# Performance work log

Hardware: AMD Instinct MI355X
Metric: run time of the kernel (lower is better)

The kernel has to match this reference:

```python
import jax, jax.numpy as jnp
import numpy as np
import math

B, S, D = 2, 1024, 1024
H = 16
HD = D // H
E = 8
DFF = 4096
EPS = 1e-5


def _ln(x, g, b):
    m = jnp.mean(x, axis=-1, keepdims=True)
    v = jnp.mean((x - m) ** 2, axis=-1, keepdims=True)
    return (x - m) / jnp.sqrt(v + EPS) * g + b


def setup_inputs() -> dict:
    key = jax.random.key(0)
    ks = jax.random.split(key, 16)
    s = 0.02
    inp = {
        'src': jax.random.normal(ks[0], (B, S, D), jnp.float32),
        'qw': jax.random.normal(ks[1], (D, D), jnp.float32) * s,
        'kw': jax.random.normal(ks[2], (D, D), jnp.float32) * s,
        'vw': jax.random.normal(ks[3], (D, D), jnp.float32) * s,
        'ow': jax.random.normal(ks[4], (D, D), jnp.float32) * s,
        'gate_w': jax.random.normal(ks[5], (D, D), jnp.float32) * s,
        'gate_b': jax.random.normal(ks[6], (D,), jnp.float32) * s,
        'scale_w': jax.random.normal(ks[7], (H, HD), jnp.float32) * s,
        'n1_g': jnp.ones((D,), jnp.float32),
        'n1_b': jnp.zeros((D,), jnp.float32),
        'n2_g': jnp.ones((D,), jnp.float32),
        'n2_b': jnp.zeros((D,), jnp.float32),
        'moe_gate_w': jax.random.normal(ks[8], (D, E), jnp.float32) * s,
        'moe_gate_b': jnp.zeros((E,), jnp.float32),
        'w1': jax.random.normal(ks[9], (E, D, DFF), jnp.float32) * s,
        'b1': jnp.zeros((E, DFF), jnp.float32),
        'ln_g': jnp.ones((E, DFF), jnp.float32),
        'ln_b': jnp.zeros((E, DFF), jnp.float32),
        'w2': jax.random.normal(ks[10], (E, DFF, D), jnp.float32) * s,
        'b2': jnp.zeros((E, D), jnp.float32),
        'res_scale': jnp.ones((E,), jnp.float32),
    }
    return inp


def _forward(src, qw, kw, vw, ow, gate_w, gate_b, scale_w, n1_g, n1_b, n2_g, n2_b,
             moe_gate_w, moe_gate_b, w1, b1, ln_g, ln_b, w2, b2, res_scale):
    # ---- MemoAttention (non-flash path, eval: no dropout, no mask) ----
    q = (src @ qw).reshape(B, S, H, HD).transpose(0, 2, 1, 3)  # [B,H,S,HD]
    k = (src @ kw).reshape(B, S, H, HD).transpose(0, 2, 1, 3)
    v = (src @ vw).reshape(B, S, H, HD).transpose(0, 2, 1, 3)
    scores = jnp.einsum('bhqd,bhkd->bhqk', q, k) / math.sqrt(HD)
    # dynamic per-(head,query) scale gate
    scale = jax.nn.sigmoid(jnp.einsum('bhsd,hd->bhs', q, scale_w)) * 2.0
    scores = scores * scale[..., None]
    attn = jax.nn.softmax(scores, axis=-1)
    out = jnp.einsum('bhqk,bhkd->bhqd', attn, v)
    out = out.transpose(0, 2, 1, 3).reshape(B, S, D)
    gate = jax.nn.sigmoid(out @ gate_w + gate_b)
    attn_out = (out * gate) @ ow

    x = _ln(src + attn_out, n1_g, n1_b)

    # ---- MoE FFN (top-2 routing; eval: no gate noise; capacity never exceeded) ----
    xf = x.reshape(-1, D)                      # [T, D]
    T = xf.shape[0]
    logits = xf @ moe_gate_w + moe_gate_b      # [T, E]
    top_v, top_i = jax.lax.top_k(logits, 2)
    # NB: original sums BOTH top-k softmax weights per token (== 1.0), and the
    wsum = jnp.sum(jax.nn.softmax(top_v, axis=-1), axis=-1)   # [T] (== 1)
    e_sel = jnp.max(top_i, axis=-1)                           # [T]
    # dense per-expert FFN on all tokens, then per-token select (masked compute)
    h = jnp.einsum('td,edf->etf', xf, w1) + b1[:, None, :]    # [E,T,DFF]
    h = _ln(h, ln_g[:, None, :], ln_b[:, None, :])
    h = jax.nn.gelu(h, approximate=False)                     # torch nn.GELU (erf)
    y = jnp.einsum('etf,efd->etd', h, w2) + b2[:, None, :]    # [E,T,D]
    y = y * res_scale[:, None, None] + xf[None]
    sel = jnp.take_along_axis(y, e_sel[None, :, None], axis=0)[0]  # [T,D]
    moe_out = (sel * wsum[:, None]).reshape(B, S, D)

    return _ln(x + moe_out, n2_g, n2_b)


def reference(src, qw, kw, vw, ow, gate_w, gate_b, scale_w, n1_g, n1_b, n2_g, n2_b,
              moe_gate_w, moe_gate_b, w1, b1, ln_g, ln_b, w2, b2, res_scale):
    return _forward(src, qw, kw, vw, ow, gate_w, gate_b, scale_w, n1_g, n1_b,
                    n2_g, n2_b, moe_gate_w, moe_gate_b, w1, b1, ln_g, ln_b,
                    w2, b2, res_scale)
```

## Files before the change

### kernel.cpp

```cpp
#include <hip/hip_runtime.h>
#include <math.h>

#define TOK    2048
#define DMODEL 1024
#define NHEAD  16
#define HDIM   64
#define NEXP   8
#define DFFN   4096

typedef unsigned short u16;
typedef __attribute__((ext_vector_type(8))) short short8;
typedef __attribute__((ext_vector_type(4))) float floatx4;

__device__ __forceinline__ float sigmoidf_(float x) { return 1.f / (1.f + __expf(-x)); }

__device__ __forceinline__ u16 f2bf(float f) {
  union { float f; unsigned u; } v; v.f = f;
  unsigned r = v.u + 0x7FFFu + ((v.u >> 16) & 1u);
  return (u16)(r >> 16);
}
__device__ __forceinline__ float bf2f(u16 h) {
  union { unsigned u; float f; } v; v.u = ((unsigned)h) << 16; return v.f;
}

__device__ __forceinline__ void gload16(const void* g, void* l) {
  __builtin_amdgcn_global_load_lds((const __attribute__((address_space(1))) void*)g,
                                   (__attribute__((address_space(3))) void*)l, 16, 0, 0);
}

__device__ __forceinline__ float blockReduceSum256(float val) {
  __shared__ float ws_[4];
  #pragma unroll
  for (int off = 32; off; off >>= 1) val += __shfl_down(val, off);
  int lane = threadIdx.x & 63, w = threadIdx.x >> 6;
  if (lane == 0) ws_[w] = val;
  __syncthreads();
  float r = ws_[0] + ws_[1] + ws_[2] + ws_[3];
  __syncthreads();
  return r;
}

__global__ __launch_bounds__(256) void prep_kernel(
    const float* __restrict__ src, u16* __restrict__ Shi, u16* __restrict__ Slo,
    const float* __restrict__ Qw, const float* __restrict__ Kw, const float* __restrict__ Vw,
    u16* __restrict__ W3h, u16* __restrict__ W3l,
    const float* __restrict__ Gw, u16* __restrict__ Gh, u16* __restrict__ Gl,
    const float* __restrict__ Ow, u16* __restrict__ Oh, u16* __restrict__ Ol,
    const float* __restrict__ W1, u16* __restrict__ W1b) {
  const int bid = blockIdx.x, tid = threadIdx.x;
  __shared__ float tile[64][65];
  if (bid < 2048) {
    const int i = bid * 256 + tid;
    const float4 v = ((const float4*)src)[i];
    const float f[4] = {v.x, v.y, v.z, v.w};
    union { u16 s[4]; uint2 u; } h, l;
    #pragma unroll
    for (int j = 0; j < 4; ++j) {
      h.s[j] = f2bf(f[j]);
      l.s[j] = f2bf(f[j] - bf2f(h.s[j]));
    }
    ((uint2*)Shi)[i] = h.u;
    ((uint2*)Slo)[i] = l.u;
    return;
  }
  if (bid < 7168) {
    const float* W; u16 *Whp, *Wlp; int n0, k0;
    if (bid < 5120) {
      const int t = bid - 2048;
      const int z = t >> 5;
      const int zz = z >> 5;
      W = (zz == 0) ? Qw : (zz == 1) ? Kw : Vw;
      Whp = W3h + (size_t)zz * DMODEL * DMODEL;
      Wlp = W3l + (size_t)zz * DMODEL * DMODEL;
      n0 = (t & 31) * 32; k0 = (z & 31) * 32;
    } else {
      const int t = bid - 5120;
      const int t2 = t & 1023;
      if (t < 1024) { W = Gw; Whp = Gh; Wlp = Gl; }
      else          { W = Ow; Whp = Oh; Wlp = Ol; }
      n0 = (t2 & 31) * 32; k0 = (t2 >> 5) * 32;
    }
    const int r = tid >> 3, c4 = (tid & 7) * 4;
    const float4 v = *(const float4*)&W[(size_t)(k0 + r) * DMODEL + n0 + c4];
    tile[r][c4+0] = v.x; tile[r][c4+1] = v.y; tile[r][c4+2] = v.z; tile[r][c4+3] = v.w;
    __syncthreads();
    union { u16 s[4]; uint2 u; } h, l;
    #pragma unroll
    for (int j = 0; j < 4; ++j) {
      const float f = tile[c4 + j][r];
      h.s[j] = f2bf(f);
      l.s[j] = f2bf(f - bf2f(h.s[j]));
    }
    *(uint2*)&Whp[(size_t)(n0 + r) * DMODEL + k0 + c4] = h.u;
    *(uint2*)&Wlp[(size_t)(n0 + r) * DMODEL + k0 + c4] = l.u;
    return;
  }
  const int bid2 = bid - 7168;
  const int e = bid2 >> 10;
  const int rem = bid2 & 1023;
  const int n0 = (rem & 63) * 64;
  const int k0 = (rem >> 6) * 64;
  const float* W = W1 + (size_t)e * DMODEL * DFFN;
  u16* O = W1b + (size_t)e * DFFN * DMODEL;
  const int r = tid >> 2, c16 = (tid & 3) * 16;
  #pragma unroll
  for (int jj = 0; jj < 4; ++jj) {
    const float4 v = *(const float4*)&W[(size_t)(k0 + r) * DFFN + n0 + c16 + jj * 4];
    tile[r][c16 + jj*4 + 0] = v.x; tile[r][c16 + jj*4 + 1] = v.y;
    tile[r][c16 + jj*4 + 2] = v.z; tile[r][c16 + jj*4 + 3] = v.w;
  }
  __syncthreads();
  union { u16 s[8]; uint4 u; } o0, o1;
  #pragma unroll
  for (int j = 0; j < 8; ++j) o0.s[j] = f2bf(tile[c16 + j][r]);
  #pragma unroll
  for (int j = 0; j < 8; ++j) o1.s[j] = f2bf(tile[c16 + 8 + j][r]);
  *(uint4*)&O[(size_t)(n0 + r) * DMODEL + k0 + c16]     = o0.u;
  *(uint4*)&O[(size_t)(n0 + r) * DMODEL + k0 + c16 + 8] = o1.u;
}

template<int EPI, int TN>
__device__ __forceinline__ void gemm_split_body(
    u16* Ah, u16* Al, u16* Bh, u16* Bl, int bx, int by,
    const u16* __restrict__ Ahi, const u16* __restrict__ Alo,
    const u16* __restrict__ Whi, const u16* __restrict__ Wlo,
    const float* __restrict__ bias, const float* __restrict__ mul,
    float* __restrict__ Cf, u16* __restrict__ Chi, u16* __restrict__ Clo,
    u16* __restrict__ Vth, u16* __restrict__ Vtl,
    int M, int N, int K) {
  constexpr int NF = TN / 32;
  const int tid = threadIdx.x;
  const int lane = tid & 63, wave = tid >> 6;
  const int row0 = by * 128, col0 = bx * TN;
  const int wm = (wave & 1) * 64, wn = (wave >> 1) * (TN / 2);
  const int mr = tid >> 3;
  const int ksrc = (tid & 7) ^ ((tid >> 3) & 7);
  const floatx4 zero = {0.f, 0.f, 0.f, 0.f};
  floatx4 acc[4][NF];
  #pragma unroll
  for (int i = 0; i < 4; ++i)
    #pragma unroll
    for (int j = 0; j < NF; ++j) acc[i][j] = zero;

  for (int k0 = 0; k0 < K; k0 += 64) {
    __syncthreads();
    #pragma unroll
    for (int p = 0; p < 4; ++p) {
      const size_t ga = (size_t)(row0 + p * 32 + mr) * K + (k0 + ksrc * 8);
      const size_t off = (size_t)(p * 256 + wave * 64) * 16;
      gload16(Ahi + ga, (char*)Ah + off);
      gload16(Alo + ga, (char*)Al + off);
    }
    #pragma unroll
    for (int p = 0; p < NF; ++p) {
      const size_t gb = (size_t)(col0 + p * 32 + mr) * K + (k0 + ksrc * 8);
      const size_t off = (size_t)(p * 256 + wave * 64) * 16;
      gload16(Whi + gb, (char*)Bh + off);
      gload16(Wlo + gb, (char*)Bl + off);
    }
    __syncthreads();
    #pragma unroll
    for (int kk = 0; kk < 2; ++kk) {
      short8 ah[4], al[4], bh[NF], bl[NF];
      #pragma unroll
      for (int i = 0; i < 4; ++i) {
        const int ml = wm + i * 16 + (lane & 15);
        const int cm = (kk * 4 + (lane >> 4)) ^ (ml & 7);
        ah[i] = *(const short8*)&Ah[ml * 64 + cm * 8];
        al[i] = *(const short8*)&Al[ml * 64 + cm * 8];
      }
      #pragma unroll
      for (int j = 0; j < NF; ++j) {
        const int nl = wn + j * 16 + (lane & 15);
        const int cn = (kk * 4 + (lane >> 4)) ^ (nl & 7);
        bh[j] = *(const short8*)&Bh[nl * 64 + cn * 8];
        bl[j] = *(const short8*)&Bl[nl * 64 + cn * 8];
      }
      #pragma unroll
      for (int i = 0; i < 4; ++i)
        #pragma unroll
        for (int j = 0; j < NF; ++j) {
          acc[i][j] = __builtin_amdgcn_mfma_f32_16x16x32_bf16(ah[i], bh[j], acc[i][j], 0, 0, 0);
          acc[i][j] = __builtin_amdgcn_mfma_f32_16x16x32_bf16(al[i], bh[j], acc[i][j], 0, 0, 0);
          acc[i][j] = __builtin_amdgcn_mfma_f32_16x16x32_bf16(ah[i], bl[j], acc[i][j], 0, 0, 0);
        }
    }
  }
  const int cl = lane & 15, quad = lane >> 4;
  if (EPI == 2 && col0 >= 2048) {
    #pragma unroll
    for (int i = 0; i < 4; ++i)
      #pragma unroll
      for (int j = 0; j < NF; ++j) {
        const int dg = col0 + wn + j * 16 + cl - 2048;
        const int bh_ = dg >> 6, d = dg & 63;
        const int row = row0 + wm + i * 16 + quad * 4;
        const int b = row >> 10, t0 = row & 1023;
        union { u16 s[4]; uint2 u; } hh, ll;
        #pragma unroll
        for (int r = 0; r < 4; ++r) {
          const float v = acc[i][j][r];
          hh.s[r] = f2bf(v);
          ll.s[r] = f2bf(v - bf2f(hh.s[r]));
        }
        const size_t base = ((size_t)(b * 16 + bh_) * 64 + d) * 1024 + t0;
        *(uint2*)&Vth[base] = hh.u;
        *(uint2*)&Vtl[base] = ll.u;
      }
    return;
  }
  #pragma unroll
  for (int i = 0; i < 4; ++i)
    #pragma unroll
    for (int j = 0; j < NF; ++j) {
      const int col = col0 + wn + j * 16 + cl;
      #pragma unroll
      for (int r = 0; r < 4; ++r) {
        const int row = row0 + wm + i * 16 + quad * 4 + r;
        const float v = acc[i][j][r];
        if (EPI == 0) {
          Cf[(size_t)row * N + col] = v;
        } else if (EPI == 1) {
          const float s = sigmoidf_(v + bias[col]);
          const float g = s * mul[(size_t)row * N + col];
          const u16 hh = f2bf(g);
          Chi[(size_t)row * N + col] = hh;
          Clo[(size_t)row * N + col] = f2bf(g - bf2f(hh));
        } else {
          const u16 hh = f2bf(v);
          Chi[(size_t)row * N + col] = hh;
          Clo[(size_t)row * N + col] = f2bf(v - bf2f(hh));
        }
      }
    }
}

template<int EPI, int TN>
__global__ __launch_bounds__(256, TN == 64 ? 3 : 2) void gemm_split_kernel(
    const u16* __restrict__ Ahi, const u16* __restrict__ Alo,
    const u16* __restrict__ Whi, const u16* __restrict__ Wlo,
    const float* __restrict__ bias, const float* __restrict__ mul,
    float* __restrict__ Cf, u16* __restrict__ Chi, u16* __restrict__ Clo,
    u16* __restrict__ Vth, u16* __restrict__ Vtl,
    int M, int N, int K) {
  __shared__ u16 Ah[128*64], Al[128*64], Bh[TN*64], Bl[TN*64];
  gemm_split_body<EPI, TN>(Ah, Al, Bh, Bl, blockIdx.x, blockIdx.y,
      Ahi, Alo, Whi, Wlo, bias, mul, Cf, Chi, Clo, Vth, Vtl, M, N, K);
}

struct GemmShared { u16 Ah[128*64]; u16 Al[128*64]; u16 Bh[64*64]; u16 Bl[64*64]; };
template<int EPI>
__global__ __launch_bounds__(256, 3) void gemm_split_w2_kernel(
    const u16* __restrict__ Ahi, const u16* __restrict__ Alo,
    const u16* __restrict__ Whi, const u16* __restrict__ Wlo,
    const float* __restrict__ bias, const float* __restrict__ mul,
    float* __restrict__ Cf, u16* __restrict__ Chi, u16* __restrict__ Clo,
    const float* __restrict__ W2, u16* __restrict__ W2b, int khalf) {
  __shared__ union { GemmShared g; float tile[32][33]; } sm;
  const int bid = blockIdx.x;
  if (bid < 256) {
    gemm_split_body<EPI, 64>(sm.g.Ah, sm.g.Al, sm.g.Bh, sm.g.Bl, bid & 15, bid >> 4,
        Ahi, Alo, Whi, Wlo, bias, mul, Cf, Chi, Clo, nullptr, nullptr,
        TOK, DMODEL, DMODEL);
    return;
  }
  const int t = bid - 256;
  const int e = t >> 5, n0 = (t & 31) * 32;
  const float* W = W2 + (size_t)e * DFFN * DMODEL;
  u16* O = W2b + (size_t)e * DMODEL * DFFN;
  const int r = threadIdx.x >> 3, c4 = (threadIdx.x & 7) * 4;
  for (int kt = 0; kt < 64; ++kt) {
    const int k0 = khalf * 2048 + kt * 32;
    __syncthreads();
    const float4 v = *(const float4*)&W[(size_t)(k0 + r) * DMODEL + n0 + c4];
    sm.tile[r][c4+0] = v.x; sm.tile[r][c4+1] = v.y;
    sm.tile[r][c4+2] = v.z; sm.tile[r][c4+3] = v.w;
    __syncthreads();
    union { u16 s[4]; uint2 u; } h4;
    #pragma unroll
    for (int j = 0; j < 4; ++j) h4.s[j] = f2bf(sm.tile[c4 + j][r]);
    *(uint2*)&O[(size_t)(n0 + r) * DFFN + k0 + c4] = h4.u;
  }
}

template<int EPI, int TN>
__global__ __launch_bounds__(256, TN == 64 ? 4 : 3) void gemm_moe_kernel(
    const u16* __restrict__ A, const u16* __restrict__ Wt,
    const float* __restrict__ bias,
    const int* __restrict__ perm, const int* __restrict__ offs,
    const int* __restrict__ counts,
    u16* __restrict__ Hout, float* __restrict__ P0, float* __restrict__ P1,
    int N, int K) {
  constexpr int NF = TN / 32;
  const int z = blockIdx.z;
  const int e = (EPI == 0) ? z : (z & 7);
  const int ks = (EPI == 0) ? 0 : (z >> 3);
  const int ne = counts[e];
  const int tm = blockIdx.y;
  if (tm * 128 >= ne) return;
  const int kbeg = (EPI == 0) ? 0 : ks * (K >> 1);
  const int kend = (EPI == 0) ? K : kbeg + (K >> 1);
  __shared__ u16 As_[128*64], Bs_[TN*64];
  __shared__ int toks[128];
  const int tid = threadIdx.x;
  if (tid < 128) {
    const int idx = tm * 128 + tid;
    toks[tid] = perm[offs[e] + (idx < ne ? idx : 0)];
  }
  __syncthreads();
  const int lane = tid & 63, wave = tid >> 6;
  const int wm = (wave & 1) * 64, wn = (wave >> 1) * (TN / 2);
  const int mr = tid >> 3;
  const int ksrc = (tid & 7) ^ ((tid >> 3) & 7);
  size_t abase[4];
  #pragma unroll
  for (int p = 0; p < 4; ++p) abase[p] = (size_t)toks[p * 32 + mr] * K;
  const u16* We = Wt + (size_t)e * N * K;
  const int col0 = blockIdx.x * TN;
  const floatx4 zero = {0.f, 0.f, 0.f, 0.f};
  floatx4 acc[4][NF];
  #pragma unroll
  for (int i = 0; i < 4; ++i)
    #pragma unroll
    for (int j = 0; j < NF; ++j) acc[i][j] = zero;

  for (int k0 = kbeg; k0 < kend; k0 += 64) {
    __syncthreads();
    #pragma unroll
    for (int p = 0; p < 4; ++p) {
      const size_t off = (size_t)(p * 256 + wave * 64) * 16;
      gload16(A + abase[p] + (k0 + ksrc * 8), (char*)As_ + off);
    }
    #pragma unroll
    for (int p = 0; p < NF; ++p) {
      const size_t off = (size_t)(p * 256 + wave * 64) * 16;
      gload16(We + (size_t)(col0 + p * 32 + mr) * K + (k0 + ksrc * 8), (char*)Bs_ + off);
    }
    __syncthreads();
    #pragma unroll
    for (int kk = 0; kk < 2; ++kk) {
      short8 a[4], b[NF];
      #pragma unroll
      for (int i = 0; i < 4; ++i) {
        const int ml = wm + i * 16 + (lane & 15);
        const int cm = (kk * 4 + (lane >> 4)) ^ (ml & 7);
        a[i] = *(const short8*)&As_[ml * 64 + cm * 8];
      }
      #pragma unroll
      for (int j = 0; j < NF; ++j) {
        const int nl = wn + j * 16 + (lane & 15);
        const int cn = (kk * 4 + (lane >> 4)) ^ (nl & 7);
        b[j] = *(const short8*)&Bs_[nl * 64 + cn * 8];
      }
      #pragma unroll
      for (int i = 0; i < 4; ++i)
        #pragma unroll
        for (int j = 0; j < NF; ++j)
          acc[i][j] = __builtin_amdgcn_mfma_f32_16x16x32_bf16(a[i], b[j], acc[i][j], 0, 0, 0);
    }
  }
  const int cl = lane & 15, quad = lane >> 4;
  float* Pp = (EPI == 1) ? (ks ? P1 : P0) : nullptr;
  #pragma unroll
  for (int i = 0; i < 4; ++i)
    #pragma unroll
    for (int j = 0; j < NF; ++j) {
      const int col = col0 + wn + j * 16 + cl;
      #pragma unroll
      for (int r = 0; r < 4; ++r) {
        const int rl = wm + i * 16 + quad * 4 + r;
        if (tm * 128 + rl < ne) {
          const int tok = toks[rl];
          if (EPI == 0)
            Hout[(size_t)tok * N + col] = f2bf(acc[i][j][r] + bias[(size_t)e * N + col]);
          else
            Pp[(size_t)tok * N + col] = acc[i][j][r];
        }
      }
    }
}

__global__ __launch_bounds__(512, 2) void attn_mfma_kernel(
    const u16* __restrict__ QKh, const u16* __restrict__ QKl,
    const u16* __restrict__ Vth, const u16* __restrict__ Vtl,
    const float* __restrict__ scale_w,
    float* __restrict__ AOf, u16* __restrict__ AOh, u16* __restrict__ AOl) {
  const int qt = blockIdx.x, h = blockIdx.y, b = blockIdx.z;
  __shared__ u16 Kh[64*64], Kl[64*64], Vh[64*64], Vl[64*64];
  __shared__ u16 Ph[8][16*40], Pl[8][16*40];
  const int tid = threadIdx.x, lane = tid & 63, wave = tid >> 6;
  const int i15 = lane & 15, quad = lane >> 4;
  const floatx4 zero = {0.f, 0.f, 0.f, 0.f};

  short8 qh[2], ql[2];
  const size_t qrow = ((size_t)b * 1024 + qt * 128 + wave * 16 + i15) * 3072 + h * 64;
  #pragma unroll
  for (int kk = 0; kk < 2; ++kk) {
    qh[kk] = *(const short8*)&QKh[qrow + kk * 32 + quad * 8];
    ql[kk] = *(const short8*)&QKl[qrow + kk * 32 + quad * 8];
  }
  float dot = 0.f;
  #pragma unroll
  for (int kk = 0; kk < 2; ++kk)
    #pragma unroll
    for (int j = 0; j < 8; ++j) {
      const float sw = scale_w[h * 64 + kk * 32 + quad * 8 + j];
      dot += (bf2f((u16)qh[kk][j]) + bf2f((u16)ql[kk][j])) * sw;
    }
  dot += __shfl_xor(dot, 16);
  dot += __shfl_xor(dot, 32);
  const float g = 2.f * sigmoidf_(dot) * 0.125f;
  float stot[4];
  #pragma unroll
  for (int r = 0; r < 4; ++r) stot[r] = __shfl(g, (lane >> 4) * 4 + r);

  float m_r[4], l_r[4];
  floatx4 Of[4];
  #pragma unroll
  for (int r = 0; r < 4; ++r) { m_r[r] = -1e30f; l_r[r] = 0.f; }
  #pragma unroll
  for (int f = 0; f < 4; ++f) Of[f] = zero;
  u16* PhW = Ph[wave];
  u16* PlW = Pl[wave];

  const int sr = tid >> 3;
  const int sc = ((tid & 7) ^ (sr & 7)) * 8;
  for (int kt = 0; kt < 16; ++kt) {
    __syncthreads();
    {
      const size_t off = (size_t)wave * 1024;
      const size_t kg = ((size_t)b * 1024 + kt * 64 + sr) * 3072 + 1024 + h * 64 + sc;
      gload16(QKh + kg, (char*)Kh + off);
      gload16(QKl + kg, (char*)Kl + off);
      const size_t vg = ((size_t)(b * 16 + h) * 64 + sr) * 1024 + kt * 64 + sc;
      gload16(Vth + vg, (char*)Vh + off);
      gload16(Vtl + vg, (char*)Vl + off);
    }
    __syncthreads();
    float pm[4][4];
    #pragma unroll
    for (int jn = 0; jn < 4; ++jn) {
      floatx4 a = zero;
      #pragma unroll
      for (int kk = 0; kk < 2; ++kk) {
        const int n = jn * 16 + i15;
        const int ch = ((kk * 4 + quad) ^ (n & 7)) * 8;
        const short8 bh = *(const short8*)&Kh[n * 64 + ch];
        const short8 bl = *(const short8*)&Kl[n * 64 + ch];
        a = __builtin_amdgcn_mfma_f32_16x16x32_bf16(qh[kk], bh, a, 0, 0, 0);
        a = __builtin_amdgcn_mfma_f32_16x16x32_bf16(ql[kk], bh, a, 0, 0, 0);
        a = __builtin_amdgcn_mfma_f32_16x16x32_bf16(qh[kk], bl, a, 0, 0, 0);
      }
      #pragma unroll
      for (int r = 0; r < 4; ++r) pm[jn][r] = a[r] * stot[r];
    }
    float alpha[4];
    #pragma unroll
    for (int r = 0; r < 4; ++r) {
      float mx = fmaxf(fmaxf(pm[0][r], pm[1][r]), fmaxf(pm[2][r], pm[3][r]));
      mx = fmaxf(mx, __shfl_xor(mx, 1));
      mx = fmaxf(mx, __shfl_xor(mx, 2));
      mx = fmaxf(mx, __shfl_xor(mx, 4));
      mx = fmaxf(mx, __shfl_xor(mx, 8));
      const float mn = fmaxf(m_r[r], mx);
      alpha[r] = __expf(m_r[r] - mn);
      m_r[r] = mn;
      float rs = 0.f;
      #pragma unroll
      for (int jn = 0; jn < 4; ++jn) { pm[jn][r] = __expf(pm[jn][r] - mn); rs += pm[jn][r]; }
      rs += __shfl_xor(rs, 1);
      rs += __shfl_xor(rs, 2);
      rs += __shfl_xor(rs, 4);
      rs += __shfl_xor(rs, 8);
      l_r[r] = l_r[r] * alpha[r] + rs;
    }
    #pragma unroll
    for (int f = 0; f < 4; ++f)
      #pragma unroll
      for (int r = 0; r < 4; ++r) Of[f][r] *= alpha[r];
    #pragma unroll
    for (int kk = 0; kk < 2; ++kk) {
      #pragma unroll
      for (int jj = 0; jj < 2; ++jj) {
        const int jn = kk * 2 + jj;
        #pragma unroll
        for (int r = 0; r < 4; ++r) {
          const int a = (quad * 4 + r) * 40 + jj * 16 + i15;
          const u16 hh = f2bf(pm[jn][r]);
          PhW[a] = hh;
          PlW[a] = f2bf(pm[jn][r] - bf2f(hh));
        }
      }
      const short8 pah = *(const short8*)&PhW[i15 * 40 + quad * 8];
      const short8 pal = *(const short8*)&PlW[i15 * 40 + quad * 8];
      #pragma unroll
      for (int f = 0; f < 4; ++f) {
        const int d = f * 16 + i15;
        const int ch = ((kk * 4 + quad) ^ (d & 7)) * 8;
        const short8 vbh = *(const short8*)&Vh[d * 64 + ch];
        const short8 vbl = *(const short8*)&Vl[d * 64 + ch];
        Of[f] = __builtin_amdgcn_mfma_f32_16x16x32_bf16(pah, vbh, Of[f], 0, 0, 0);
        Of[f] = __builtin_amdgcn_mfma_f32_16x16x32_bf16(pal, vbh, Of[f], 0, 0, 0);
        Of[f] = __builtin_amdgcn_mfma_f32_16x16x32_bf16(pah, vbl, Of[f], 0, 0, 0);
      }
    }
  }
  float inv[4];
  #pragma unroll
  for (int r = 0; r < 4; ++r) inv[r] = 1.f / l_r[r];
  #pragma unroll
  for (int f = 0; f < 4; ++f)
    #pragma unroll
    for (int r = 0; r < 4; ++r) {
      const size_t row = (size_t)b * 1024 + qt * 128 + wave * 16 + quad * 4 + r;
      const int col = h * 64 + f * 16 + i15;
      const float val = Of[f][r] * inv[r];
      AOf[row * 1024 + col] = val;
      const u16 hh = f2bf(val);
      AOh[row * 1024 + col] = hh;
      AOl[row * 1024 + col] = f2bf(val - bf2f(hh));
    }
}

__global__ __launch_bounds__(256) void ln_add_router_kernel(
    const float* __restrict__ A, const float* __restrict__ Bp,
    const float* __restrict__ g, const float* __restrict__ beta,
    float* __restrict__ outf, u16* __restrict__ outh,
    const float* __restrict__ gw, const float* __restrict__ gb,
    int* __restrict__ e_sel) {
  __shared__ float xrow[DMODEL];
  int t = blockIdx.x, tid = threadIdx.x;
  const float* a = A + (size_t)t * DMODEL;
  const float* b = Bp + (size_t)t * DMODEL;
  float v[4]; float s = 0.f;
  #pragma unroll
  for (int i = 0; i < 4; ++i) { int d = tid + i*256; v[i] = a[d] + b[d]; s += v[i]; }
  s = blockReduceSum256(s);
  float mean = s * (1.f/1024.f);
  float q = 0.f;
  #pragma unroll
  for (int i = 0; i < 4; ++i) { float df = v[i]-mean; q += df*df; }
  q = blockReduceSum256(q);
  float rstd = rsqrtf(q*(1.f/1024.f) + 1e-5f);
  #pragma unroll
  for (int i = 0; i < 4; ++i) {
    int d = tid + i*256;
    float val = (v[i]-mean)*rstd*g[d] + beta[d];
    outf[(size_t)t*DMODEL + d] = val;
    outh[(size_t)t*DMODEL + d] = f2bf(val);
    xrow[d] = val;
  }
  __syncthreads();
  if (tid < 64) {
    float acc[NEXP] = {};
    for (int d = tid; d < DMODEL; d += 64) {
      float xv = xrow[d];
      const float* gr = gw + (size_t)d * NEXP;
      #pragma unroll
      for (int e = 0; e < NEXP; ++e) acc[e] += xv * gr[e];
    }
    #pragma unroll
    for (int e = 0; e < NEXP; ++e) {
      #pragma unroll
      for (int off = 32; off; off >>= 1) acc[e] += __shfl_down(acc[e], off);
    }
    if (tid == 0) {
      float lg[NEXP];
      #pragma unroll
      for (int e = 0; e < NEXP; ++e) lg[e] = acc[e] + gb[e];
      int i1 = 0;
      for (int e = 1; e < NEXP; ++e) if (lg[e] > lg[i1]) i1 = e;
      int i2 = -1;
      for (int e = 0; e < NEXP; ++e) {
        if (e == i1) continue;
        if (i2 < 0 || lg[e] > lg[i2]) i2 = e;
      }
      e_sel[t] = (i1 > i2) ? i1 : i2;
    }
  }
}

__global__ __launch_bounds__(256) void ln_final_kernel(
    const float* __restrict__ X, const float* __restrict__ P0,
    const float* __restrict__ P1, const float* __restrict__ B2,
    const float* __restrict__ rsv, const int* __restrict__ e_sel,
    const float* __restrict__ g, const float* __restrict__ beta,
    float* __restrict__ out) {
  int t = blockIdx.x, tid = threadIdx.x;
  const int e = e_sel[t];
  const float rse = rsv[e];
  const float* b2e = B2 + (size_t)e * DMODEL;
  const int d0 = tid * 4;
  const size_t base = (size_t)t * DMODEL + d0;
  const float4 xv = *(const float4*)&X[base];
  const float4 p0v = *(const float4*)&P0[base];
  const float4 p1v = *(const float4*)&P1[base];
  const float4 bv = *(const float4*)&b2e[d0];
  float v[4]; float s = 0.f;
  v[0] = 2.f*xv.x + (p0v.x + p1v.x + bv.x) * rse;
  v[1] = 2.f*xv.y + (p0v.y + p1v.y + bv.y) * rse;
  v[2] = 2.f*xv.z + (p0v.z + p1v.z + bv.z) * rse;
  v[3] = 2.f*xv.w + (p0v.w + p1v.w + bv.w) * rse;
  s = v[0] + v[1] + v[2] + v[3];
  s = blockReduceSum256(s);
  float mean = s * (1.f/1024.f);
  float q = 0.f;
  #pragma unroll
  for (int i = 0; i < 4; ++i) { float df = v[i]-mean; q += df*df; }
  q = blockReduceSum256(q);
  float rstd = rsqrtf(q*(1.f/1024.f) + 1e-5f);
  const float4 g4 = *(const float4*)&g[d0];
  const float4 be4 = *(const float4*)&beta[d0];
  float4 o;
  o.x = (v[0]-mean)*rstd*g4.x + be4.x;
  o.y = (v[1]-mean)*rstd*g4.y + be4.y;
  o.z = (v[2]-mean)*rstd*g4.z + be4.z;
  o.w = (v[3]-mean)*rstd*g4.w + be4.w;
  *(float4*)&out[base] = o;
}

__global__ __launch_bounds__(256) void moe_group_kernel(
    const int* __restrict__ e_sel, int* __restrict__ perm,
    int* __restrict__ g_offs, int* __restrict__ g_counts) {
  __shared__ int cnt[NEXP], offs[NEXP], cur[NEXP];
  int tid = threadIdx.x;
  if (tid < NEXP) cnt[tid] = 0;
  __syncthreads();
  for (int t = tid; t < TOK; t += 256) atomicAdd(&cnt[e_sel[t]], 1);
  __syncthreads();
  if (tid == 0) {
    int run = 0;
    for (int e = 0; e < NEXP; ++e) { offs[e] = run; cur[e] = run; run += cnt[e]; }
  }
  __syncthreads();
  if (tid < NEXP) { g_offs[tid] = offs[tid]; g_counts[tid] = cnt[tid]; }
  for (int t = tid; t < TOK; t += 256) {
    int pos = atomicAdd(&cur[e_sel[t]], 1);
    perm[pos] = t;
  }
}

__global__ __launch_bounds__(256) void moe_ln_gelu_kernel(
    u16* __restrict__ H, const float* __restrict__ ln_g,
    const float* __restrict__ ln_b, const int* __restrict__ e_sel) {
  int t = blockIdx.x, tid = threadIdx.x;
  int e = e_sel[t];
  u16* hp = H + (size_t)t * DFFN;
  float v[16]; float s = 0.f;
  #pragma unroll
  for (int i = 0; i < 4; ++i) {
    const int d = i * 1024 + tid * 4;
    union { uint2 u; u16 q[4]; } hv;
    hv.u = *(const uint2*)&hp[d];
    #pragma unroll
    for (int j = 0; j < 4; ++j) { v[i*4+j] = bf2f(hv.q[j]); s += v[i*4+j]; }
  }
  s = blockReduceSum256(s);
  float mean = s * (1.f/4096.f);
  float q = 0.f;
  #pragma unroll
  for (int i = 0; i < 16; ++i) { float df = v[i]-mean; q += df*df; }
  q = blockReduceSum256(q);
  float rstd = rsqrtf(q*(1.f/4096.f) + 1e-5f);
  const float* gg = ln_g + (size_t)e * DFFN;
  const float* bb = ln_b + (size_t)e * DFFN;
  #pragma unroll
  for (int i = 0; i < 4; ++i) {
    const int d = i * 1024 + tid * 4;
    const float4 g4 = *(const float4*)&gg[d];
    const float4 b4 = *(const float4*)&bb[d];
    const float gf[4] = {g4.x, g4.y, g4.z, g4.w};
    const float bf[4] = {b4.x, b4.y, b4.z, b4.w};
    union { uint2 u; u16 q[4]; } ov;
    #pragma unroll
    for (int j = 0; j < 4; ++j) {
      float xx = (v[i*4+j]-mean)*rstd*gf[j] + bf[j];
      ov.q[j] = f2bf(0.5f * xx * (1.f + erff(xx * 0.7071067811865475f)));
    }
    *(uint2*)&hp[d] = ov.u;
  }
}

extern "C" void kernel_launch(void* const* d_in, const int* in_sizes, int n_in,
                              void* d_out, int out_size, void* d_ws, size_t ws_size,
                              hipStream_t stream) {
  (void)in_sizes; (void)n_in; (void)out_size; (void)ws_size;
  const float* src    = (const float*)d_in[0];
  const float* qw     = (const float*)d_in[1];
  const float* kw     = (const float*)d_in[2];
  const float* vw     = (const float*)d_in[3];
  const float* ow     = (const float*)d_in[4];
  const float* gate_w = (const float*)d_in[5];
  const float* gate_b = (const float*)d_in[6];
  const float* scale_w= (const float*)d_in[7];
  const float* n1_g   = (const float*)d_in[8];
  const float* n1_b   = (const float*)d_in[9];
  const float* n2_g   = (const float*)d_in[10];
  const float* n2_b   = (const float*)d_in[11];
  const float* mgw    = (const float*)d_in[12];
  const float* mgb    = (const float*)d_in[13];
  const float* w1     = (const float*)d_in[14];
  const float* b1     = (const float*)d_in[15];
  const float* ln_g   = (const float*)d_in[16];
  const float* ln_b   = (const float*)d_in[17];
  const float* w2     = (const float*)d_in[18];
  const float* b2     = (const float*)d_in[19];
  const float* rs     = (const float*)d_in[20];

  char* ws = (char*)d_ws;
  const size_t MB = 1024 * 1024;
  u16*   src_hi = (u16*)(ws + 0*MB);
  u16*   src_lo = (u16*)(ws + 4*MB);
  u16*   Wt3_hi = (u16*)(ws + 8*MB);
  u16*   Wt3_lo = (u16*)(ws + 14*MB);
  u16*   gw_hi  = (u16*)(ws + 20*MB);
  u16*   gw_lo  = (u16*)(ws + 22*MB);
  u16*   ow_hi  = (u16*)(ws + 24*MB);
  u16*   ow_lo  = (u16*)(ws + 26*MB);
  u16*   W1A    = (u16*)(ws + 28*MB);
  u16*   W2A    = (u16*)(ws + 92*MB);
  u16*   qkv_hi = (u16*)(ws + 156*MB);
  u16*   qkv_lo = (u16*)(ws + 168*MB);
  u16*   Vt_hi  = (u16*)(ws + 180*MB);
  u16*   Vt_lo  = (u16*)(ws + 184*MB);
  float* ao     = (float*)(ws + 188*MB);
  u16*   ao_hi  = (u16*)(ws + 196*MB);
  u16*   ao_lo  = (u16*)(ws + 200*MB);
  u16*   gb_hi  = (u16*)(ws + 204*MB);
  u16*   gb_lo  = (u16*)(ws + 208*MB);
  float* proj   = (float*)(ws + 212*MB);
  float* x      = (float*)(ws + 220*MB);
  u16*   x_hi   = (u16*)(ws + 228*MB);
  u16*   h      = (u16*)(ws + 232*MB);
  float* p0     = (float*)(ws + 248*MB);
  float* p1     = (float*)(ws + 256*MB);
  int*   e_sel  = (int*)(ws + 264*MB);
  int*   perm   = e_sel + TOK;
  int*   offs   = perm + TOK;
  int*   cnts   = offs + NEXP;

  dim3 blk(256);

  prep_kernel<<<15360, blk, 0, stream>>>(src, src_hi, src_lo,
      qw, kw, vw, Wt3_hi, Wt3_lo, gate_w, gw_hi, gw_lo, ow, ow_hi, ow_lo,
      w1, W1A);

  gemm_split_kernel<2,64><<<dim3(48,16), blk, 0, stream>>>(src_hi, src_lo,
      Wt3_hi, Wt3_lo, nullptr, nullptr, nullptr, qkv_hi, qkv_lo, Vt_hi, Vt_lo,
      TOK, 3072, DMODEL);

  attn_mfma_kernel<<<dim3(8, NHEAD, 2), dim3(512), 0, stream>>>(
      qkv_hi, qkv_lo, Vt_hi, Vt_lo, scale_w, ao, ao_hi, ao_lo);

  gemm_split_w2_kernel<1><<<512, blk, 0, stream>>>(ao_hi, ao_lo, gw_hi, gw_lo,
      gate_b, ao, nullptr, gb_hi, gb_lo, w2, W2A, 0);

  gemm_split_w2_kernel<0><<<512, blk, 0, stream>>>(gb_hi, gb_lo, ow_hi, ow_lo,
      nullptr, nullptr, proj, nullptr, nullptr, w2, W2A, 1);

  ln_add_router_kernel<<<TOK, blk, 0, stream>>>(src, proj, n1_g, n1_b, x, x_hi,
      mgw, mgb, e_sel);

  moe_group_kernel<<<1, blk, 0, stream>>>(e_sel, perm, offs, cnts);

  gemm_moe_kernel<0,128><<<dim3(DFFN/128, 16, 8), blk, 0, stream>>>(
      x_hi, W1A, b1, perm, offs, cnts, h, nullptr, nullptr, DFFN, DMODEL);

  moe_ln_gelu_kernel<<<TOK, blk, 0, stream>>>(h, ln_g, ln_b, e_sel);

  gemm_moe_kernel<1,64><<<dim3(DMODEL/64, 16, 16), blk, 0, stream>>>(
      h, W2A, nullptr, perm, offs, cnts, nullptr, p0, p1, DMODEL, DFFN);

  ln_final_kernel<<<TOK, blk, 0, stream>>>(x, p0, p1, b2, rs, e_sel, n2_g, n2_b,
      (float*)d_out);
}
```

Baseline: 713.3 us.

## Shrink gate/out-proj GEMM tiles to 64x64 and retile W1 transpose

Templates the split-bf16 GEMM body on the M tile and uses 64x64 tiles for the gate and output projection GEMMs. This doubles their block count to 512 (768 including the fused W2 conversion blocks), which improves CU fill on a 2048x1024 output. It also raises the launch bound to 4 blocks per CU and sets the QKV GEMM bound to 3. Separately, it reorganises the W1 transpose/convert blocks so global reads are row-coalesced and writes are 16-byte stores per thread. Smaller tiles reduce data reuse per block, and the tighter launch bounds may force register spilling.

```diff
diff --git a/kernel.cpp b/kernel.cpp
--- a/kernel.cpp
+++ b/kernel.cpp
@@ -102,24 +102,32 @@
   const int k0 = (rem >> 6) * 64;
   const float* W = W1 + (size_t)e * DMODEL * DFFN;
   u16* O = W1b + (size_t)e * DFFN * DMODEL;
-  const int r = tid >> 2, c16 = (tid & 3) * 16;
-  #pragma unroll
-  for (int jj = 0; jj < 4; ++jj) {
-    const float4 v = *(const float4*)&W[(size_t)(k0 + r) * DFFN + n0 + c16 + jj * 4];
-    tile[r][c16 + jj*4 + 0] = v.x; tile[r][c16 + jj*4 + 1] = v.y;
-    tile[r][c16 + jj*4 + 2] = v.z; tile[r][c16 + jj*4 + 3] = v.w;
+  {
+    const int lr = tid >> 4;
+    const int lc = (tid & 15) * 4;
+    #pragma unroll
+    for (int p = 0; p < 4; ++p) {
+      const float4 v = *(const float4*)&W[(size_t)(k0 + p * 16 + lr) * DFFN + n0 + lc];
+      tile[p*16 + lr][lc+0] = v.x; tile[p*16 + lr][lc+1] = v.y;
+      tile[p*16 + lr][lc+2] = v.z; tile[p*16 + lr][lc+3] = v.w;
+    }
   }
   __syncthreads();
-  union { u16 s[8]; uint4 u; } o0, o1;
-  #pragma unroll
-  for (int j = 0; j < 8; ++j) o0.s[j] = f2bf(tile[c16 + j][r]);
-  #pragma unroll
-  for (int j = 0; j < 8; ++j) o1.s[j] = f2bf(tile[c16 + 8 + j][r]);
-  *(uint4*)&O[(size_t)(n0 + r) * DMODEL + k0 + c16]     = o0.u;
-  *(uint4*)&O[(size_t)(n0 + r) * DMODEL + k0 + c16 + 8] = o1.u;
-}
-
-template<int EPI, int TN>
+  {
+    const int kl = (tid & 7) * 8;
+    const int nl = tid >> 3;
+    #pragma unroll
+    for (int q = 0; q < 2; ++q) {
+      const int n = q * 32 + nl;
+      union { u16 s[8]; uint4 u; } o;
+      #pragma unroll
+      for (int j = 0; j < 8; ++j) o.s[j] = f2bf(tile[kl + j][n]);
+      *(uint4*)&O[(size_t)(n0 + n) * DMODEL + k0 + kl] = o.u;
+    }
+  }
+}
+
+template<int EPI, int TM, int TN>
 __device__ __forceinline__ void gemm_split_body(
     u16* Ah, u16* Al, u16* Bh, u16* Bl, int bx, int by,
     const u16* __restrict__ Ahi, const u16* __restrict__ Alo,
@@ -128,24 +136,25 @@
     float* __restrict__ Cf, u16* __restrict__ Chi, u16* __restrict__ Clo,
     u16* __restrict__ Vth, u16* __restrict__ Vtl,
     int M, int N, int K) {
+  constexpr int MI = TM / 32;
   constexpr int NF = TN / 32;
   const int tid = threadIdx.x;
   const int lane = tid & 63, wave = tid >> 6;
-  const int row0 = by * 128, col0 = bx * TN;
-  const int wm = (wave & 1) * 64, wn = (wave >> 1) * (TN / 2);
+  const int row0 = by * TM, col0 = bx * TN;
+  const int wm = (wave & 1) * (TM / 2), wn = (wave >> 1) * (TN / 2);
   const int mr = tid >> 3;
   const int ksrc = (tid & 7) ^ ((tid >> 3) & 7);
   const floatx4 zero = {0.f, 0.f, 0.f, 0.f};
-  floatx4 acc[4][NF];
-  #pragma unroll
-  for (int i = 0; i < 4; ++i)
+  floatx4 acc[MI][NF];
+  #pragma unroll
+  for (int i = 0; i < MI; ++i)
     #pragma unroll
     for (int j = 0; j < NF; ++j) acc[i][j] = zero;
 
   for (int k0 = 0; k0 < K; k0 += 64) {
     __syncthreads();
     #pragma unroll
-    for (int p = 0; p < 4; ++p) {
+    for (int p = 0; p < MI; ++p) {
       const size_t ga = (size_t)(row0 + p * 32 + mr) * K + (k0 + ksrc * 8);
       const size_t off = (size_t)(p * 256 + wave * 64) * 16;
       gload16(Ahi + ga, (char*)Ah + off);
@@ -161,9 +170,9 @@
     __syncthreads();
     #pragma unroll
     for (int kk = 0; kk < 2; ++kk) {
-      short8 ah[4], al[4], bh[NF], bl[NF];
-      #pragma unroll
-      for (int i = 0; i < 4; ++i) {
+      short8 ah[MI], al[MI], bh[NF], bl[NF];
+      #pragma unroll
+      for (int i = 0; i < MI; ++i) {
         const int ml = wm + i * 16 + (lane & 15);
         const int cm = (kk * 4 + (lane >> 4)) ^ (ml & 7);
         ah[i] = *(const short8*)&Ah[ml * 64 + cm * 8];
@@ -177,7 +186,7 @@
         bl[j] = *(const short8*)&Bl[nl * 64 + cn * 8];
       }
       #pragma unroll
-      for (int i = 0; i < 4; ++i)
+      for (int i = 0; i < MI; ++i)
         #pragma unroll
         for (int j = 0; j < NF; ++j) {
           acc[i][j] = __builtin_amdgcn_mfma_f32_16x16x32_bf16(ah[i], bh[j], acc[i][j], 0, 0, 0);
@@ -189,7 +198,7 @@
   const int cl = lane & 15, quad = lane >> 4;
   if (EPI == 2 && col0 >= 2048) {
     #pragma unroll
-    for (int i = 0; i < 4; ++i)
+    for (int i = 0; i < MI; ++i)
       #pragma unroll
       for (int j = 0; j < NF; ++j) {
         const int dg = col0 + wn + j * 16 + cl - 2048;
@@ -210,7 +219,7 @@
     return;
   }
   #pragma unroll
-  for (int i = 0; i < 4; ++i)
+  for (int i = 0; i < MI; ++i)
     #pragma unroll
     for (int j = 0; j < NF; ++j) {
       const int col = col0 + wn + j * 16 + cl;
@@ -236,7 +245,7 @@
 }
 
 template<int EPI, int TN>
-__global__ __launch_bounds__(256, TN == 64 ? 3 : 2) void gemm_split_kernel(
+__global__ __launch_bounds__(256, 3) void gemm_split_kernel(
     const u16* __restrict__ Ahi, const u16* __restrict__ Alo,
     const u16* __restrict__ Whi, const u16* __restrict__ Wlo,
     const float* __restrict__ bias, const float* __restrict__ mul,
@@ -244,27 +253,28 @@
     u16* __restrict__ Vth, u16* __restrict__ Vtl,
     int M, int N, int K) {
   __shared__ u16 Ah[128*64], Al[128*64], Bh[TN*64], Bl[TN*64];
-  gemm_split_body<EPI, TN>(Ah, Al, Bh, Bl, blockIdx.x, blockIdx.y,
+  gemm_split_body<EPI, 128, TN>(Ah, Al, Bh, Bl, blockIdx.x, blockIdx.y,
       Ahi, Alo, Whi, Wlo, bias, mul, Cf, Chi, Clo, Vth, Vtl, M, N, K);
 }
 
-struct GemmShared { u16 Ah[128*64]; u16 Al[128*64]; u16 Bh[64*64]; u16 Bl[64*64]; };
+struct GemmShared64 { u16 Ah[64*64]; u16 Al[64*64]; u16 Bh[64*64]; u16 Bl[64*64]; };
 template<int EPI>
-__global__ __launch_bounds__(256, 3) void gemm_split_w2_kernel(
+__global__ __launch_bounds__(256, 4) void gemm_split_w2_kernel(
     const u16* __restrict__ Ahi, const u16* __restrict__ Alo,
     const u16* __restrict__ Whi, const u16* __restrict__ Wlo,
     const float* __restrict__ bias, const float* __restrict__ mul,
     float* __restrict__ Cf, u16* __restrict__ Chi, u16* __restrict__ Clo,
     const float* __restrict__ W2, u16* __restrict__ W2b, int khalf) {
-  __shared__ union { GemmShared g; float tile[32][33]; } sm;
+  __shared__ union { GemmShared64 g; float tile[32][33]; } sm;
   const int bid = blockIdx.x;
-  if (bid < 256) {
-    gemm_split_body<EPI, 64>(sm.g.Ah, sm.g.Al, sm.g.Bh, sm.g.Bl, bid & 15, bid >> 4,
+  if (bid < 512) {
+    gemm_split_body<EPI, 64, 64>(sm.g.Ah, sm.g.Al, sm.g.Bh, sm.g.Bl,
+        bid & 15, bid >> 4,
         Ahi, Alo, Whi, Wlo, bias, mul, Cf, Chi, Clo, nullptr, nullptr,
         TOK, DMODEL, DMODEL);
     return;
   }
-  const int t = bid - 256;
+  const int t = bid - 512;
   const int e = t >> 5, n0 = (t & 31) * 32;
   const float* W = W2 + (size_t)e * DFFN * DMODEL;
   u16* O = W2b + (size_t)e * DMODEL * DFFN;
@@ -752,10 +762,10 @@
   attn_mfma_kernel<<<dim3(8, NHEAD, 2), dim3(512), 0, stream>>>(
       qkv_hi, qkv_lo, Vt_hi, Vt_lo, scale_w, ao, ao_hi, ao_lo);
 
-  gemm_split_w2_kernel<1><<<512, blk, 0, stream>>>(ao_hi, ao_lo, gw_hi, gw_lo,
+  gemm_split_w2_kernel<1><<<768, blk, 0, stream>>>(ao_hi, ao_lo, gw_hi, gw_lo,
       gate_b, ao, nullptr, gb_hi, gb_lo, w2, W2A, 0);
 
-  gemm_split_w2_kernel<0><<<512, blk, 0, stream>>>(gb_hi, gb_lo, ow_hi, ow_lo,
+  gemm_split_w2_kernel<0><<<768, blk, 0, stream>>>(gb_hi, gb_lo, ow_hi, ow_lo,
       nullptr, nullptr, proj, nullptr, nullptr, w2, W2A, 1);
 
   ln_add_router_kernel<<<TOK, blk, 0, stream>>>(src, proj, n1_g, n1_b, x, x_hi,
```

Measured after the change: 699.4 us. About the same (-1.9%).
